# Kernel optimization log

Measured on AMD Instinct MI355X. Metric: run time of the kernel, lower is better.

## Reference

```python
import jax, jax.numpy as jnp
import numpy as np
import math

B, S, HID = 2, 2048, 1024
NH = 16
HD = HID // NH          # 64
VD = HD // 2            # 32 value dim
TD = HD - VD            # 32 type dim
EPS = 1e-6


def setup_inputs() -> dict:
    key = jax.random.key(0)
    ks = jax.random.split(key, 12)
    std = 1.0 / math.sqrt(HID)
    xav = math.sqrt(6.0 / (TD + TD))
    return {
        "x": jax.random.normal(ks[0], (B, S, HID), dtype=jnp.float32),
        "q_w": jax.random.uniform(ks[1], (HID, HID), jnp.float32, -std, std),
        "q_b": jax.random.uniform(ks[2], (HID,), jnp.float32, -std, std),
        "k_w": jax.random.uniform(ks[3], (HID, HID), jnp.float32, -std, std),
        "k_b": jax.random.uniform(ks[4], (HID,), jnp.float32, -std, std),
        "v_w": jax.random.uniform(ks[5], (HID, HID), jnp.float32, -std, std),
        "v_b": jax.random.uniform(ks[6], (HID,), jnp.float32, -std, std),
        "out_w": jax.random.uniform(ks[7], (HID, HID), jnp.float32, -std, std),
        "out_b": jax.random.uniform(ks[8], (HID,), jnp.float32, -std, std),
        "type_bilinear": jax.random.uniform(ks[9], (NH, TD, TD), jnp.float32, -xav, xav),
        "type_bias": jnp.full((NH,), 2.0, dtype=jnp.float32),
        "mask": jnp.ones((B, S), dtype=jnp.int32),
    }


def reference(x, q_w, q_b, k_w, k_b, v_w, v_b, out_w, out_b, type_bilinear, type_bias, mask):
    # projections: [B,S,HID] -> [B,NH,S,HD]
    def proj(w, b):
        y = jnp.einsum("bsi,io->bso", x, w) + b
        return y.reshape(B, S, NH, HD).transpose(0, 2, 1, 3)

    q = proj(q_w, q_b)
    k = proj(k_w, k_b)
    v = proj(v_w, v_b)

    q_val, q_type = q[..., :VD], q[..., VD:]
    k_val, k_type = k[..., :VD], k[..., VD:]

    # standard value score: [B,NH,S,S]
    val_scores = jnp.einsum("bhqd,bhkd->bhqk", q_val, k_val) / math.sqrt(VD)

    # per-head bilinear type score: q_type @ W_h @ k_type^T + bias_h
    qt = jnp.einsum("bhqd,hde->bhqe", q_type, type_bilinear)
    type_scores = jnp.einsum("bhqe,bhke->bhqk", qt, k_type) + type_bias[None, :, None, None]
    type_unif = jax.nn.sigmoid(type_scores)

    scores = val_scores + jnp.log(type_unif + EPS)

    # mask: [B,S] -> broadcast over heads and query dim (keys masked)
    m = (mask[:, None, None, :] != 0)
    scores = jnp.where(m, scores, -jnp.inf)

    attn = jax.nn.softmax(scores, axis=-1)
    out = jnp.einsum("bhqk,bhkd->bhqd", attn, v)          # [B,NH,S,HD]
    out = out.transpose(0, 2, 1, 3).reshape(B, S, HID)
    return jnp.einsum("bsi,io->bso", out, out_w) + out_b
```

## Files before the change

kernel.cpp:

```cpp
#include <hip/hip_runtime.h>
#include <hip/hip_bf16.h>
#include <math.h>

typedef __attribute__((ext_vector_type(8))) short bf16x8;
typedef __attribute__((ext_vector_type(4))) float f32x4;
typedef __attribute__((ext_vector_type(4))) int   i32x4;

#define NHh 16
#define Sq  2048
#define HIDq 1024
#define HDq 64
#define LOG2E 1.4426950408889634f

#if __has_builtin(__builtin_amdgcn_exp2f)
#define EXP2F(x) __builtin_amdgcn_exp2f(x)
#else
#define EXP2F(x) exp2f(x)
#endif
#if __has_builtin(__builtin_amdgcn_rcpf)
#define RCPF(x) __builtin_amdgcn_rcpf(x)
#else
#define RCPF(x) (1.0f/(x))
#endif

__device__ __forceinline__ unsigned short f2bf(float f){
  union { float f; unsigned u; } v; v.f = f;
  unsigned r = v.u + 0x7fffu + ((v.u >> 16) & 1u);
  return (unsigned short)(r >> 16);
}
__device__ __forceinline__ float bf2f(unsigned short s){
  union { unsigned u; float f; } v; v.u = ((unsigned)s) << 16;
  return v.f;
}
__device__ __forceinline__ unsigned pk2bf(float lo, float hi){
  union { __hip_bfloat162 h; unsigned u; } w;
  w.h = __float22bfloat162_rn(make_float2(lo, hi));
  return w.u;
}

__device__ __forceinline__ void gload_lds16(const unsigned short* g, unsigned short* l){
  __builtin_amdgcn_global_load_lds(
      (const __attribute__((address_space(1))) unsigned int*)g,
      (__attribute__((address_space(3))) unsigned int*)l, 16, 0, 0);
}

__global__ __launch_bounds__(256) void convert_x(const float* __restrict__ in,
                                                 unsigned short* __restrict__ out, int n8,
                                                 const int* __restrict__ mask,
                                                 float* __restrict__ Mf){
  int bid = blockIdx.x;
  int nmain = gridDim.x - 2;
  if (bid >= nmain){
    int base = (bid - nmain)*2048 + threadIdx.x*8;
    #pragma unroll
    for (int j=0;j<8;j++) Mf[base+j] = mask[base+j] ? 0.f : -1e30f;
    return;
  }
  int i = bid*256 + threadIdx.x;
  if (i >= n8) return;
  const f32x4* p = (const f32x4*)(in + (size_t)i*8);
  f32x4 a = p[0], b = p[1];
  union { unsigned short us[8]; i32x4 v; } o;
  #pragma unroll
  for (int j=0;j<4;j++){ o.us[j] = f2bf(a[j]); o.us[4+j] = f2bf(b[j]); }
  *(i32x4*)(out + (size_t)i*8) = o.v;
}

__global__ __launch_bounds__(256) void transpose_w(const float* __restrict__ w0, const float* __restrict__ w1,
                                                   const float* __restrict__ w2, const float* __restrict__ w3,
                                                   unsigned short* __restrict__ wT){
  __shared__ float tile[32][33];
  int z = blockIdx.z;
  const float* w = (z==0)?w0:(z==1)?w1:(z==2)?w2:w3;
  unsigned short* dst = wT + (size_t)z*HIDq*HIDq;
  int tx = threadIdx.x, ty = threadIdx.y;
  int n0 = blockIdx.x*32, k0 = blockIdx.y*32;
  #pragma unroll
  for (int i=ty;i<32;i+=8) tile[i][tx] = w[(size_t)(k0+i)*HIDq + n0+tx];
  __syncthreads();
  #pragma unroll
  for (int i=ty;i<32;i+=8) dst[(size_t)(n0+i)*HIDq + k0+tx] = f2bf(tile[tx][i]);
}

__device__ __forceinline__ void gemm_core_gl(const unsigned short* __restrict__ Ag,
                                             const unsigned short* __restrict__ Bg,
                                             unsigned short* As, unsigned short* Bs,
                                             int t, int wv, int lane, int wr, int wc, int lr, int g,
                                             f32x4 acc[4][4]){
  for (int k0=0; k0<HIDq; k0+=64){
    __syncthreads();
    #pragma unroll
    for (int j=0;j<4;j++){
      int flat = (j*4+wv)*64 + lane;
      int row = flat>>3, c = flat&7;
      int srcc = (c ^ (row&7))*8;
      gload_lds16(Ag + (size_t)row*HIDq + k0 + srcc, &As[flat*8]);
      gload_lds16(Bg + (size_t)row*HIDq + k0 + srcc, &Bs[flat*8]);
    }
    __syncthreads();
    #pragma unroll
    for (int ks=0; ks<2; ks++){
      bf16x8 af[4], bfv[4];
      #pragma unroll
      for (int m=0;m<4;m++){
        int rr = wr + m*16 + lr;
        af[m]  = *(bf16x8*)&As[rr*64 + (((ks*4+g) ^ (rr&7))*8)];
      }
      #pragma unroll
      for (int n=0;n<4;n++){
        int rr = wc + n*16 + lr;
        bfv[n] = *(bf16x8*)&Bs[rr*64 + (((ks*4+g) ^ (rr&7))*8)];
      }
      #pragma unroll
      for (int n=0;n<4;n++)
        #pragma unroll
        for (int m=0;m<4;m++)
          acc[n][m] = __builtin_amdgcn_mfma_f32_16x16x32_bf16(bfv[n], af[m], acc[n][m], 0,0,0);
    }
  }
}

__global__ __launch_bounds__(256) void gemm_qkv(const unsigned short* __restrict__ xbf,
    const unsigned short* __restrict__ wT,
    const float* __restrict__ q_b, const float* __restrict__ k_b, const float* __restrict__ v_b,
    unsigned short* __restrict__ Qeff, unsigned short* __restrict__ Keff,
    unsigned short* __restrict__ Vt){
  __shared__ unsigned short As[128*64];
  __shared__ unsigned short Bs[128*64];
  const int t = threadIdx.x;
  const int wv = t>>6, lane = t&63, g = lane>>4, lr = lane&15;
  const int wr = (wv>>1)*64, wc = (wv&1)*64;
  f32x4 acc[4][4] = {};
  const int xb = blockIdx.x, yb = blockIdx.y;
  const float VS = 0.25501335f;

  if (xb < 16){
    const int row0 = yb*128, col0 = xb*128;
    gemm_core_gl(xbf + (size_t)row0*HIDq, wT + (size_t)col0*HIDq, As, Bs, t, wv, lane, wr, wc, lr, g, acc);
    #pragma unroll
    for (int n=0;n<4;n++){
      #pragma unroll
      for (int m=0;m<4;m++){
        int row = row0 + wr + m*16 + lr;
        int b_ = row>>11, ss = row&2047;
        int colb = col0 + wc + n*16 + g*4;
        int seg = colb>>10, cw = colb&1023;
        int hh = cw>>6, d = cw&63;
        const float* bp = seg ? k_b : q_b;
        f32x4 bb = *(const f32x4*)&bp[cw];
        float sc = seg ? 1.0f : (d < 32 ? VS : -LOG2E);
        unsigned short* E = seg ? Keff : Qeff;
        float v0 = (acc[n][m][0]+bb[0])*sc, v1 = (acc[n][m][1]+bb[1])*sc;
        float v2 = (acc[n][m][2]+bb[2])*sc, v3 = (acc[n][m][3]+bb[3])*sc;
        union { unsigned u[2]; unsigned long long ll; } W;
        W.u[0] = pk2bf(v0,v1); W.u[1] = pk2bf(v2,v3);
        *(unsigned long long*)&E[(((size_t)b_*NHh+hh)*Sq+ss)*HDq + d] = W.ll;
      }
    }
  } else {
    const int row0 = (xb-16)*128, col0 = yb*128;
    gemm_core_gl(wT + (size_t)2*HIDq*HIDq + (size_t)row0*HIDq, xbf + (size_t)col0*HIDq,
                 As, Bs, t, wv, lane, wr, wc, lr, g, acc);
    #pragma unroll
    for (int n=0;n<4;n++){
      #pragma unroll
      for (int m=0;m<4;m++){
        int chan = row0 + wr + m*16 + lr;
        int hh = chan>>6, d = chan&63;
        float bv = v_b[chan];
        int colb = col0 + wc + n*16 + g*4;
        int b_ = colb>>11, ss = colb&2047;
        union { unsigned u[2]; unsigned long long ll; } W;
        W.u[0] = pk2bf(acc[n][m][0]+bv, acc[n][m][1]+bv);
        W.u[1] = pk2bf(acc[n][m][2]+bv, acc[n][m][3]+bv);
        *(unsigned long long*)&Vt[(((size_t)b_*NHh+hh)*HDq + d)*Sq + ss] = W.ll;
      }
    }
  }
}

__global__ __launch_bounds__(256) void gemm_out(const unsigned short* __restrict__ A,
                                                const unsigned short* __restrict__ Bt,
                                                const float* __restrict__ bias,
                                                float* __restrict__ C){
  __shared__ unsigned short As[128*64];
  __shared__ unsigned short Bs[128*64];
  const int t = threadIdx.x;
  const int wv = t>>6, lane = t&63, g = lane>>4, lr = lane&15;
  const int wr = (wv>>1)*64, wc = (wv&1)*64;
  const int row0 = blockIdx.y*128, col0 = blockIdx.x*128;
  f32x4 acc[4][4] = {};
  gemm_core_gl(A + (size_t)row0*HIDq, Bt + (size_t)col0*HIDq, As, Bs, t, wv, lane, wr, wc, lr, g, acc);
  #pragma unroll
  for (int n=0;n<4;n++){
    #pragma unroll
    for (int m=0;m<4;m++){
      int row = row0 + wr + m*16 + lr;
      int colb = col0 + wc + n*16 + g*4;
      f32x4 bb = *(const f32x4*)&bias[colb];
      f32x4 o = acc[n][m] + bb;
      *(f32x4*)&C[(size_t)row*HIDq + colb] = o;
    }
  }
}

__global__ __launch_bounds__(256,4) void attn_kernel(
    const unsigned short* __restrict__ Qe, const unsigned short* __restrict__ Ke,
    const unsigned short* __restrict__ Vt, const float* __restrict__ Tb,
    const float* __restrict__ tbias, const float* __restrict__ Mf,
    unsigned short* __restrict__ Obuf)
{
  __shared__ __align__(16) unsigned char smem[40960];
  unsigned short* Ks0 = (unsigned short*)smem;
  unsigned short* Ks1 = (unsigned short*)(smem + 8192);
  unsigned short* Vs0 = (unsigned short*)(smem + 16384);
  unsigned short* Vs1 = (unsigned short*)(smem + 24576);
  unsigned short* Pl  = (unsigned short*)(smem + 32768);
  float* qls = (float*)smem;
  unsigned short* qtls = Pl;

  const int t = threadIdx.x;
  const int dd = blockIdx.x;
  const int slot = dd>>3, xcd = dd&7;
  const int x = slot & 31;
  const int bh = ((slot>>5)<<3) | xcd;
  const int h = bh & 15, b = bh >> 4;
  const int q0 = x*64;
  const int wv = t>>6, lane = t&63, g = lane>>4, lr = lane&15;

  const unsigned short* Qb  = Qe + (((size_t)b*NHh+h)*Sq + q0)*HDq;
  const unsigned short* Kb  = Ke + ((size_t)b*NHh+h)*(size_t)Sq*HDq;
  const unsigned short* Vtb = Vt + ((size_t)b*NHh+h)*(size_t)HDq*Sq;
  const float* Mfb = Mf + (size_t)b*Sq;

  {
    int row = t>>2, c8 = (t&3)*8;
    bf16x8 v = *(const bf16x8*)(Qb + (size_t)row*HDq + 32 + c8);
    #pragma unroll
    for (int j=0;j<8;j++) qls[row*33 + c8 + j] = bf2f((unsigned short)v[j]);
  }
  __syncthreads();
  {
    int row = t&63, e0 = (t>>6)*8;
    const float* Th = Tb + (size_t)h*1024;
    float a[8] = {};
    #pragma unroll 4
    for (int d=0; d<32; d++){
      float qd = qls[row*33 + d];
      const f32x4* tp = (const f32x4*)(Th + d*32 + e0);
      f32x4 t0 = tp[0], t1 = tp[1];
      a[0]+=qd*t0[0]; a[1]+=qd*t0[1]; a[2]+=qd*t0[2]; a[3]+=qd*t0[3];
      a[4]+=qd*t1[0]; a[5]+=qd*t1[1]; a[6]+=qd*t1[2]; a[7]+=qd*t1[3];
    }
    union { unsigned u[2]; unsigned long long ll; } W0, W1;
    W0.u[0]=pk2bf(a[0],a[1]); W0.u[1]=pk2bf(a[2],a[3]);
    W1.u[0]=pk2bf(a[4],a[5]); W1.u[1]=pk2bf(a[6],a[7]);
    *(unsigned long long*)&qtls[row*40 + e0]     = W0.ll;
    *(unsigned long long*)&qtls[row*40 + e0 + 4] = W1.ll;
  }
  bf16x8 qvf = *(const bf16x8*)(Qb + (size_t)(wv*16+lr)*HDq + g*8);
  __syncthreads();
  bf16x8 qtn = *(const bf16x8*)&qtls[(wv*16+lr)*40 + g*8];

  #pragma unroll
  for (int i=0;i<2;i++){
    int c = t + i*256;
    int kr = c>>3, kc = c&7;
    gload_lds16(Kb + (size_t)kr*HDq + ((kc ^ (kr&7))*8), Ks0 + c*8);
    int vd = c>>3, vc = c&7;
    gload_lds16(Vtb + (size_t)vd*Sq + ((vc ^ (vd&7))*8), Vs0 + c*8);
  }
  __syncthreads();

  const float tbn = -tbias[h]*LOG2E;
  const f32x4 tbc = {tbn,tbn,tbn,tbn};
  f32x4 oT[4] = {};
  f32x4 lsum = {0.f,0.f,0.f,0.f};
  unsigned short* Pw = &Pl[wv*1024 + lr*64];
  const int swp = (lr&7)*8;
  bf16x8 onesf;
  #pragma unroll
  for (int j=0;j<8;j++) onesf[j] = (short)0x3F80;

  auto phase = [&](const unsigned short* Kc, const unsigned short* Vc, int key0,
                   bool doStage, int key0n, unsigned short* Kn, unsigned short* Vn){
    f32x4 madd[4];
    #pragma unroll
    for (int ks=0; ks<4; ks++)
      madd[ks] = *(const f32x4*)(Mfb + key0 + ks*16 + g*4);
    if (doStage){
      #pragma unroll
      for (int i=0;i<2;i++){
        int c = t + i*256;
        int kr = c>>3, kc = c&7;
        gload_lds16(Kb + (size_t)(key0n+kr)*HDq + ((kc ^ (kr&7))*8), Kn + c*8);
        int vd = c>>3, vc = c&7;
        gload_lds16(Vtb + (size_t)vd*Sq + key0n + ((vc ^ (vd&7))*8), Vn + c*8);
      }
    }
    f32x4 sv[4], st[4];
    __builtin_amdgcn_s_setprio(1);
    #pragma unroll
    for (int ks=0; ks<4; ks++){
      const unsigned short* kb = Kc + (ks*16+lr)*64;
      bf16x8 kf0 = *(const bf16x8*)(kb + (((g  ) ^ (lr&7))*8));
      bf16x8 kf1 = *(const bf16x8*)(kb + (((4+g) ^ (lr&7))*8));
      sv[ks] = __builtin_amdgcn_mfma_f32_16x16x32_bf16(kf0, qvf, madd[ks], 0,0,0);
      st[ks] = __builtin_amdgcn_mfma_f32_16x16x32_bf16(kf1, qtn, tbc, 0,0,0);
    }
    __builtin_amdgcn_s_setprio(0);
    #pragma unroll
    for (int ks=0; ks<4; ks++){
      float p0 = EXP2F(sv[ks][0]) * RCPF(1.f + EXP2F(st[ks][0]));
      float p1 = EXP2F(sv[ks][1]) * RCPF(1.f + EXP2F(st[ks][1]));
      float p2 = EXP2F(sv[ks][2]) * RCPF(1.f + EXP2F(st[ks][2]));
      float p3 = EXP2F(sv[ks][3]) * RCPF(1.f + EXP2F(st[ks][3]));
      union { unsigned u[2]; unsigned long long ll; } W;
      W.u[0] = pk2bf(p0,p1); W.u[1] = pk2bf(p2,p3);
      *(unsigned long long*)(Pw + ((ks*16 + g*4) ^ swp)) = W.ll;
    }
    #pragma unroll
    for (int ks2=0; ks2<2; ks2++){
      bf16x8 pf = *(const bf16x8*)(Pw + ((ks2*32 + g*8) ^ swp));
      __builtin_amdgcn_s_setprio(1);
      lsum = __builtin_amdgcn_mfma_f32_16x16x32_bf16(onesf, pf, lsum, 0,0,0);
      #pragma unroll
      for (int db=0; db<4; db++){
        bf16x8 vf = *(const bf16x8*)(Vc + (db*16+lr)*64 + (((ks2*4+g) ^ (lr&7))*8));
        oT[db] = __builtin_amdgcn_mfma_f32_16x16x32_bf16(vf, pf, oT[db], 0,0,0);
      }
      __builtin_amdgcn_s_setprio(0);
    }
  };

  for (int kt=0; kt<Sq; kt+=128){
    phase(Ks0, Vs0, kt,      true,           kt+64,  Ks1, Vs1);
    __syncthreads();
    phase(Ks1, Vs1, kt+64,   kt+128 < Sq,    kt+128, Ks0, Vs0);
    __syncthreads();
  }

  float linv = (lsum[0] > 0.f) ? RCPF(lsum[0]) : 0.f;
  int srow = q0 + wv*16 + lr;
  unsigned short* Ob = Obuf + ((size_t)b*Sq + srow)*HIDq + h*HDq;
  #pragma unroll
  for (int db=0; db<4; db++){
    union { unsigned u[2]; unsigned long long ll; } W;
    W.u[0] = pk2bf(oT[db][0]*linv, oT[db][1]*linv);
    W.u[1] = pk2bf(oT[db][2]*linv, oT[db][3]*linv);
    *(unsigned long long*)(Ob + db*16 + g*4) = W.ll;
  }
}

extern "C" void kernel_launch(void* const* d_in, const int* in_sizes, int n_in,
                              void* d_out, int out_size, void* d_ws, size_t ws_size,
                              hipStream_t stream) {
  const float* x     = (const float*)d_in[0];
  const float* q_w   = (const float*)d_in[1];
  const float* q_b   = (const float*)d_in[2];
  const float* k_w   = (const float*)d_in[3];
  const float* k_b   = (const float*)d_in[4];
  const float* v_w   = (const float*)d_in[5];
  const float* v_b   = (const float*)d_in[6];
  const float* out_w = (const float*)d_in[7];
  const float* out_b = (const float*)d_in[8];
  const float* Tb    = (const float*)d_in[9];
  const float* tbias = (const float*)d_in[10];
  const int*   mask  = (const int*)d_in[11];

  const size_t MROWS = 4096;
  unsigned short* xbf  = (unsigned short*)d_ws;
  unsigned short* wT   = xbf  + MROWS*HIDq;
  unsigned short* Qeff = wT   + (size_t)4*HIDq*HIDq;
  unsigned short* Keff = Qeff + MROWS*HIDq;
  unsigned short* Vt   = Keff + MROWS*HIDq;
  unsigned short* Obuf = Vt   + MROWS*HIDq;
  float*          Mf   = (float*)(Obuf + MROWS*HIDq);

  int n8 = (int)(MROWS*HIDq/8);
  convert_x<<<dim3(n8/256 + 2), dim3(256), 0, stream>>>(x, xbf, n8, mask, Mf);
  transpose_w<<<dim3(32,32,4), dim3(32,8), 0, stream>>>(q_w, k_w, v_w, out_w, wT);

  gemm_qkv<<<dim3(24,32), dim3(256), 0, stream>>>(xbf, wT, q_b, k_b, v_b, Qeff, Keff, Vt);

  attn_kernel<<<dim3(1024), dim3(256), 0, stream>>>(Qeff, Keff, Vt, Tb, tbias, Mf, Obuf);

  gemm_out<<<dim3(8,32), dim3(256), 0, stream>>>(Obuf, wT + (size_t)3*HIDq*HIDq, out_b, (float*)d_out);
}
```

Measured before the change: 160.3 us.

## Keep attention probabilities in registers using 16x16x16 MFMA and fold mask into V

Instead of writing the probability tile P to LDS and reading it back as a B operand, the kernel now feeds the per-lane P fragments straight into 16x16x16 bf16 MFMAs as the A operand. This produces a transposed output layout and requires scalar bf16 stores at the end. Masking moves out of the score MFMA. It is applied by zeroing masked V columns in gemm_qkv and by using a bf16 mask vector as the B operand of the row-sum MFMA. This removes the LDS round trip for P and the 8KB P buffer, at the cost of twice as many smaller MFMAs, an extra barrier, and narrow uncoalesced output stores.

```diff
diff --git a/kernel.cpp b/kernel.cpp
--- a/kernel.cpp
+++ b/kernel.cpp
@@ -3,6 +3,7 @@
 #include <math.h>
 
 typedef __attribute__((ext_vector_type(8))) short bf16x8;
+typedef __attribute__((ext_vector_type(4))) short bf16x4;
 typedef __attribute__((ext_vector_type(4))) float f32x4;
 typedef __attribute__((ext_vector_type(4))) int   i32x4;
 
@@ -23,6 +24,18 @@
 #define RCPF(x) (1.0f/(x))
 #endif
 
+#if __has_builtin(__builtin_amdgcn_mfma_f32_16x16x16bf16_1k)
+__device__ __forceinline__ f32x4 MFMA16(bf16x4 a, bf16x4 b, f32x4 c){
+  return __builtin_amdgcn_mfma_f32_16x16x16bf16_1k(a, b, c, 0, 0, 0);
+}
+#else
+__device__ __forceinline__ f32x4 MFMA16(bf16x4 a, bf16x4 b, f32x4 c){
+  asm volatile("v_mfma_f32_16x16x16_bf16 %0, %1, %2, %0\n\ts_nop 7\n\ts_nop 7"
+               : "+v"(c) : "v"(a), "v"(b));
+  return c;
+}
+#endif
+
 __device__ __forceinline__ unsigned short f2bf(float f){
   union { float f; unsigned u; } v; v.f = f;
   unsigned r = v.u + 0x7fffu + ((v.u >> 16) & 1u);
@@ -47,13 +60,13 @@
 __global__ __launch_bounds__(256) void convert_x(const float* __restrict__ in,
                                                  unsigned short* __restrict__ out, int n8,
                                                  const int* __restrict__ mask,
-                                                 float* __restrict__ Mf){
+                                                 unsigned short* __restrict__ Mbf){
   int bid = blockIdx.x;
   int nmain = gridDim.x - 2;
   if (bid >= nmain){
     int base = (bid - nmain)*2048 + threadIdx.x*8;
     #pragma unroll
-    for (int j=0;j<8;j++) Mf[base+j] = mask[base+j] ? 0.f : -1e30f;
+    for (int j=0;j<8;j++) Mbf[base+j] = mask[base+j] ? (unsigned short)0x3F80 : (unsigned short)0;
     return;
   }
   int i = bid*256 + threadIdx.x;
@@ -123,6 +136,7 @@
 __global__ __launch_bounds__(256) void gemm_qkv(const unsigned short* __restrict__ xbf,
     const unsigned short* __restrict__ wT,
     const float* __restrict__ q_b, const float* __restrict__ k_b, const float* __restrict__ v_b,
+    const int* __restrict__ mask,
     unsigned short* __restrict__ Qeff, unsigned short* __restrict__ Keff,
     unsigned short* __restrict__ Vt){
   __shared__ unsigned short As[128*64];
@@ -170,9 +184,11 @@
         float bv = v_b[chan];
         int colb = col0 + wc + n*16 + g*4;
         int b_ = colb>>11, ss = colb&2047;
+        i32x4 mk = *(const i32x4*)&mask[(size_t)b_*Sq + ss];
+        float m0 = mk[0]?1.f:0.f, m1 = mk[1]?1.f:0.f, m2 = mk[2]?1.f:0.f, m3 = mk[3]?1.f:0.f;
         union { unsigned u[2]; unsigned long long ll; } W;
-        W.u[0] = pk2bf(acc[n][m][0]+bv, acc[n][m][1]+bv);
-        W.u[1] = pk2bf(acc[n][m][2]+bv, acc[n][m][3]+bv);
+        W.u[0] = pk2bf((acc[n][m][0]+bv)*m0, (acc[n][m][1]+bv)*m1);
+        W.u[1] = pk2bf((acc[n][m][2]+bv)*m2, (acc[n][m][3]+bv)*m3);
         *(unsigned long long*)&Vt[(((size_t)b_*NHh+hh)*HDq + d)*Sq + ss] = W.ll;
       }
     }
@@ -207,17 +223,16 @@
 __global__ __launch_bounds__(256,4) void attn_kernel(
     const unsigned short* __restrict__ Qe, const unsigned short* __restrict__ Ke,
     const unsigned short* __restrict__ Vt, const float* __restrict__ Tb,
-    const float* __restrict__ tbias, const float* __restrict__ Mf,
+    const float* __restrict__ tbias, const unsigned short* __restrict__ Mbf,
     unsigned short* __restrict__ Obuf)
 {
-  __shared__ __align__(16) unsigned char smem[40960];
+  __shared__ __align__(16) unsigned char smem[32768];
   unsigned short* Ks0 = (unsigned short*)smem;
   unsigned short* Ks1 = (unsigned short*)(smem + 8192);
   unsigned short* Vs0 = (unsigned short*)(smem + 16384);
   unsigned short* Vs1 = (unsigned short*)(smem + 24576);
-  unsigned short* Pl  = (unsigned short*)(smem + 32768);
   float* qls = (float*)smem;
-  unsigned short* qtls = Pl;
+  unsigned short* qtls = Vs0;
 
   const int t = threadIdx.x;
   const int dd = blockIdx.x;
@@ -231,7 +246,7 @@
   const unsigned short* Qb  = Qe + (((size_t)b*NHh+h)*Sq + q0)*HDq;
   const unsigned short* Kb  = Ke + ((size_t)b*NHh+h)*(size_t)Sq*HDq;
   const unsigned short* Vtb = Vt + ((size_t)b*NHh+h)*(size_t)HDq*Sq;
-  const float* Mfb = Mf + (size_t)b*Sq;
+  const unsigned short* Mbfb = Mbf + (size_t)b*Sq;
 
   {
     int row = t>>2, c8 = (t&3)*8;
@@ -261,6 +276,7 @@
   bf16x8 qvf = *(const bf16x8*)(Qb + (size_t)(wv*16+lr)*HDq + g*8);
   __syncthreads();
   bf16x8 qtn = *(const bf16x8*)&qtls[(wv*16+lr)*40 + g*8];
+  __syncthreads();
 
   #pragma unroll
   for (int i=0;i<2;i++){
@@ -274,20 +290,12 @@
 
   const float tbn = -tbias[h]*LOG2E;
   const f32x4 tbc = {tbn,tbn,tbn,tbn};
+  const f32x4 zf = {0.f,0.f,0.f,0.f};
   f32x4 oT[4] = {};
   f32x4 lsum = {0.f,0.f,0.f,0.f};
-  unsigned short* Pw = &Pl[wv*1024 + lr*64];
-  const int swp = (lr&7)*8;
-  bf16x8 onesf;
-  #pragma unroll
-  for (int j=0;j<8;j++) onesf[j] = (short)0x3F80;
 
   auto phase = [&](const unsigned short* Kc, const unsigned short* Vc, int key0,
                    bool doStage, int key0n, unsigned short* Kn, unsigned short* Vn){
-    f32x4 madd[4];
-    #pragma unroll
-    for (int ks=0; ks<4; ks++)
-      madd[ks] = *(const f32x4*)(Mfb + key0 + ks*16 + g*4);
     if (doStage){
       #pragma unroll
       for (int i=0;i<2;i++){
@@ -305,29 +313,30 @@
       const unsigned short* kb = Kc + (ks*16+lr)*64;
       bf16x8 kf0 = *(const bf16x8*)(kb + (((g  ) ^ (lr&7))*8));
       bf16x8 kf1 = *(const bf16x8*)(kb + (((4+g) ^ (lr&7))*8));
-      sv[ks] = __builtin_amdgcn_mfma_f32_16x16x32_bf16(kf0, qvf, madd[ks], 0,0,0);
+      sv[ks] = __builtin_amdgcn_mfma_f32_16x16x32_bf16(kf0, qvf, zf, 0,0,0);
       st[ks] = __builtin_amdgcn_mfma_f32_16x16x32_bf16(kf1, qtn, tbc, 0,0,0);
     }
     __builtin_amdgcn_s_setprio(0);
+    bf16x4 pa[4];
     #pragma unroll
     for (int ks=0; ks<4; ks++){
       float p0 = EXP2F(sv[ks][0]) * RCPF(1.f + EXP2F(st[ks][0]));
       float p1 = EXP2F(sv[ks][1]) * RCPF(1.f + EXP2F(st[ks][1]));
       float p2 = EXP2F(sv[ks][2]) * RCPF(1.f + EXP2F(st[ks][2]));
       float p3 = EXP2F(sv[ks][3]) * RCPF(1.f + EXP2F(st[ks][3]));
-      union { unsigned u[2]; unsigned long long ll; } W;
-      W.u[0] = pk2bf(p0,p1); W.u[1] = pk2bf(p2,p3);
-      *(unsigned long long*)(Pw + ((ks*16 + g*4) ^ swp)) = W.ll;
-    }
-    #pragma unroll
-    for (int ks2=0; ks2<2; ks2++){
-      bf16x8 pf = *(const bf16x8*)(Pw + ((ks2*32 + g*8) ^ swp));
+      union { unsigned u[2]; bf16x4 v; } P_;
+      P_.u[0] = pk2bf(p0,p1); P_.u[1] = pk2bf(p2,p3);
+      pa[ks] = P_.v;
+    }
+    #pragma unroll
+    for (int ks=0; ks<4; ks++){
+      bf16x4 mfr = *(const bf16x4*)(Mbfb + key0 + ks*16 + g*4);
       __builtin_amdgcn_s_setprio(1);
-      lsum = __builtin_amdgcn_mfma_f32_16x16x32_bf16(onesf, pf, lsum, 0,0,0);
+      lsum = MFMA16(pa[ks], mfr, lsum);
       #pragma unroll
       for (int db=0; db<4; db++){
-        bf16x8 vf = *(const bf16x8*)(Vc + (db*16+lr)*64 + (((ks2*4+g) ^ (lr&7))*8));
-        oT[db] = __builtin_amdgcn_mfma_f32_16x16x32_bf16(vf, pf, oT[db], 0,0,0);
+        bf16x4 vf = *(const bf16x4*)(Vc + (db*16+lr)*64 + (((2*ks + (g>>1)) ^ (lr&7))*8 + 4*(g&1)));
+        oT[db] = MFMA16(pa[ks], vf, oT[db]);
       }
       __builtin_amdgcn_s_setprio(0);
     }
@@ -340,15 +349,15 @@
     __syncthreads();
   }
 
-  float linv = (lsum[0] > 0.f) ? RCPF(lsum[0]) : 0.f;
-  int srow = q0 + wv*16 + lr;
-  unsigned short* Ob = Obuf + ((size_t)b*Sq + srow)*HIDq + h*HDq;
+  float linv[4];
+  #pragma unroll
+  for (int r=0;r<4;r++) linv[r] = (lsum[r] > 0.f) ? RCPF(lsum[r]) : 0.f;
+  unsigned short* Ob = Obuf + ((size_t)b*Sq + (q0 + wv*16 + g*4))*HIDq + h*HDq + lr;
   #pragma unroll
   for (int db=0; db<4; db++){
-    union { unsigned u[2]; unsigned long long ll; } W;
-    W.u[0] = pk2bf(oT[db][0]*linv, oT[db][1]*linv);
-    W.u[1] = pk2bf(oT[db][2]*linv, oT[db][3]*linv);
-    *(unsigned long long*)(Ob + db*16 + g*4) = W.ll;
+    #pragma unroll
+    for (int r=0;r<4;r++)
+      Ob[(size_t)r*HIDq + db*16] = f2bf(oT[db][r]*linv[r]);
   }
 }
 
@@ -375,15 +384,15 @@
   unsigned short* Keff = Qeff + MROWS*HIDq;
   unsigned short* Vt   = Keff + MROWS*HIDq;
   unsigned short* Obuf = Vt   + MROWS*HIDq;
-  float*          Mf   = (float*)(Obuf + MROWS*HIDq);
+  unsigned short* Mbf  = Obuf + MROWS*HIDq;
 
   int n8 = (int)(MROWS*HIDq/8);
-  convert_x<<<dim3(n8/256 + 2), dim3(256), 0, stream>>>(x, xbf, n8, mask, Mf);
+  convert_x<<<dim3(n8/256 + 2), dim3(256), 0, stream>>>(x, xbf, n8, mask, Mbf);
   transpose_w<<<dim3(32,32,4), dim3(32,8), 0, stream>>>(q_w, k_w, v_w, out_w, wT);
 
-  gemm_qkv<<<dim3(24,32), dim3(256), 0, stream>>>(xbf, wT, q_b, k_b, v_b, Qeff, Keff, Vt);
-
-  attn_kernel<<<dim3(1024), dim3(256), 0, stream>>>(Qeff, Keff, Vt, Tb, tbias, Mf, Obuf);
+  gemm_qkv<<<dim3(24,32), dim3(256), 0, stream>>>(xbf, wT, q_b, k_b, v_b, mask, Qeff, Keff, Vt);
+
+  attn_kernel<<<dim3(1024), dim3(256), 0, stream>>>(Qeff, Keff, Vt, Tb, tbias, Mbf, Obuf);
 
   gemm_out<<<dim3(8,32), dim3(256), 0, stream>>>(Obuf, wT + (size_t)3*HIDq*HIDq, out_b, (float*)d_out);
 }
```

Result: no change. 158.9 us (-0.9%).
